# Kernel optimization log

Hardware: AMD Instinct MI355X
Metric: run time of the kernel (lower is better)

## Reference

```python
import jax, jax.numpy as jnp
import numpy as np

B, N, K = 2, 8192, 16
C_IN, C_OUT, HID = 64, 256, 256
L, HEADS, DKQV = 2, 8, 32
D = HEADS * DKQV  # 256


def setup_inputs() -> dict:
    key = jax.random.key(0)
    ks = jax.random.split(key, 20)
    s = 0.02
    inp = {
        "xyzs": jax.random.normal(ks[0], (B, N, 3), jnp.float32),
        "features": jax.random.normal(ks[1], (B, N, C_IN), jnp.float32),
        "k_graph": jax.random.randint(ks[2], (B, N, K), 0, N),
        "W_in": jax.random.normal(ks[3], (C_IN, HID), jnp.float32) * s,
        "b_in": jnp.zeros((HID,), jnp.float32),
        "Wq": jax.random.normal(ks[4], (L, HID, D), jnp.float32) * s,
        "bq": jnp.zeros((L, D), jnp.float32),
        "Wk": jax.random.normal(ks[5], (L, HID, D), jnp.float32) * s,
        "bk": jnp.zeros((L, D), jnp.float32),
        "Wv": jax.random.normal(ks[6], (L, HID, D), jnp.float32) * s,
        "bv": jnp.zeros((L, D), jnp.float32),
        "Wp": jax.random.normal(ks[7], (L, 3, D), jnp.float32) * s,
        "bp": jnp.zeros((L, D), jnp.float32),
        "Wo": jax.random.normal(ks[8], (L, D, HID), jnp.float32) * s,
        "bo": jnp.zeros((L, HID), jnp.float32),
        "W_out": jax.random.normal(ks[9], (HID, C_OUT), jnp.float32) * s,
        "b_out": jnp.zeros((C_OUT,), jnp.float32),
    }
    return inp


def _gather(f, idx):
    # f: [B,N,D], idx: [B,N,K] -> [B,N,K,D]
    return jnp.take_along_axis(f[:, None], idx[..., None], axis=2)


def _knn_attn(xyz, f, idx, Wq, bq, Wk, bk, Wv, bv, Wp, bp, Wo, bo):
    b, n, _ = f.shape
    q = f @ Wq + bq                      # [B,N,D]
    k = f @ Wk + bk
    v = f @ Wv + bv
    k_nb = _gather(k, idx)               # [B,N,K,D]
    v_nb = _gather(v, idx)
    rel = xyz[:, :, None, :] - _gather(xyz, idx)   # [B,N,K,3]
    pos = rel @ Wp + bp                  # [B,N,K,D] relative positional encoding
    kh = (k_nb + pos).reshape(b, n, K, HEADS, DKQV)
    vh = (v_nb + pos).reshape(b, n, K, HEADS, DKQV)
    qh = q.reshape(b, n, HEADS, DKQV)
    logits = jnp.einsum('bnhd,bnkhd->bnhk', qh, kh) / np.sqrt(DKQV)
    attn = jax.nn.softmax(logits, axis=-1)          # softmax over K neighbors
    o = jnp.einsum('bnhk,bnkhd->bnhd', attn, vh).reshape(b, n, D)
    return o @ Wo + bo


def reference(xyzs, features, k_graph, W_in, b_in, Wq, bq, Wk, bk, Wv, bv,
              Wp, bp, Wo, bo, W_out, b_out):
    f = features @ W_in + b_in
    for l in range(L):
        res = f  # res_connection=True
        f = _knn_attn(xyzs, f, k_graph, Wq[l], bq[l], Wk[l], bk[l],
                      Wv[l], bv[l], Wp[l], bp[l], Wo[l], bo[l]) + res
    out = f @ W_out + b_out
    return jax.nn.leaky_relu(out, negative_slope=0.01)
```

## Files before the change

### kernel.cpp

```cpp
#include <hip/hip_runtime.h>
#include <hip/hip_bf16.h>

typedef __attribute__((ext_vector_type(8))) short bf16x8;
typedef __attribute__((ext_vector_type(4))) float f32x4;
typedef unsigned int uint;

constexpr int NPTS = 8192;
constexpr int BPTS = 16384;
constexpr int KNN  = 16;

__device__ __forceinline__ void gload16(const void* g, void* l) {
    __builtin_amdgcn_global_load_lds(
        (const __attribute__((address_space(1))) unsigned int*)g,
        (__attribute__((address_space(3))) unsigned int*)l, 16, 0, 0);
}

__device__ __forceinline__ float2 bf2f2(uint u) {
    float2 r;
    r.x = __uint_as_float(u << 16);
    r.y = __uint_as_float(u & 0xffff0000u);
    return r;
}

__device__ __forceinline__ uint packbf2(float a, float b) {
    union { __hip_bfloat16 h; unsigned short u; } ua, ub;
    ua.h = __float2bfloat16(a); ub.h = __float2bfloat16(b);
    return (uint)ua.u | ((uint)ub.u << 16);
}

template<int KD, bool RES, bool OUTF32, bool LRELU>
__global__ __launch_bounds__(256) void gemm_mfma(
    const __hip_bfloat16* __restrict__ A,
    const __hip_bfloat16* __restrict__ Bt,
    const float* __restrict__ b0, const float* __restrict__ b1,
    const float* __restrict__ b2,
    const __hip_bfloat16* __restrict__ res,
    void* __restrict__ Cout, int M, int N)
{
    __shared__ __align__(16) __hip_bfloat16 As[128 * 64];
    __shared__ __align__(16) __hip_bfloat16 Bs[128 * 64];

    const int tid  = threadIdx.x;
    const int lane = tid & 63;
    const int wid  = tid >> 6;
    const int wm   = (wid >> 1) * 64;
    const int wn   = (wid & 1) * 64;
    const int bm   = blockIdx.y * 128;
    const int bn   = blockIdx.x * 128;

    const int srow8 = lane >> 3;
    const int sslot = (lane & 7) ^ srow8;

    const int r = lane & 15;
    const int g = lane >> 4;

    f32x4 acc[4][4] = {};

    for (int k0 = 0; k0 < KD; k0 += 64) {
        #pragma unroll
        for (int p = 0; p < 4; ++p) {
            const int rowA = p * 32 + wid * 8 + srow8;
            gload16(&A[(size_t)(bm + rowA) * KD + k0 + sslot * 8],
                    (char*)As + (p * 32 + wid * 8) * 128);
            gload16(&Bt[(size_t)(bn + rowA) * KD + k0 + sslot * 8],
                    (char*)Bs + (p * 32 + wid * 8) * 128);
        }
        __syncthreads();

        bf16x8 af[2][4], bfr[2][4];
        #pragma unroll
        for (int s = 0; s < 2; ++s) {
            const int physA = (s * 4 + g) ^ (r & 7);
            #pragma unroll
            for (int mi = 0; mi < 4; ++mi)
                af[s][mi] = *(const bf16x8*)((const char*)As + (wm + mi * 16 + r) * 128 + physA * 16);
            #pragma unroll
            for (int ni = 0; ni < 4; ++ni)
                bfr[s][ni] = *(const bf16x8*)((const char*)Bs + (wn + ni * 16 + r) * 128 + physA * 16);
        }
        #pragma unroll
        for (int s = 0; s < 2; ++s)
            #pragma unroll
            for (int mi = 0; mi < 4; ++mi)
                #pragma unroll
                for (int ni = 0; ni < 4; ++ni)
                    acc[mi][ni] = __builtin_amdgcn_mfma_f32_16x16x32_bf16(
                        af[s][mi], bfr[s][ni], acc[mi][ni], 0, 0, 0);
        __syncthreads();
    }

    #pragma unroll
    for (int ni = 0; ni < 4; ++ni) {
        const int col = bn + wn + ni * 16 + r;
        const float* bsel = (col < 256) ? b0 : (col < 512 ? b1 : b2);
        const float bias = bsel[col & 255];
        #pragma unroll
        for (int mi = 0; mi < 4; ++mi) {
            #pragma unroll
            for (int q = 0; q < 4; ++q) {
                const int row = bm + wm + mi * 16 + g * 4 + q;
                float v = acc[mi][ni][q] + bias;
                if (RES)  v += __bfloat162float(res[(size_t)row * N + col]);
                if (LRELU) v = v > 0.f ? v : 0.01f * v;
                if (OUTF32) ((float*)Cout)[(size_t)row * N + col] = v;
                else ((__hip_bfloat16*)Cout)[(size_t)row * N + col] = __float2bfloat16(v);
            }
        }
    }
}

__global__ __launch_bounds__(256) void prep_kernel(
    const float* __restrict__ W_in, const float* __restrict__ Wq,
    const float* __restrict__ Wk,  const float* __restrict__ Wv,
    const float* __restrict__ Wo,  const float* __restrict__ W_out,
    const float* __restrict__ features,
    __hip_bfloat16* __restrict__ WtIn,  __hip_bfloat16* __restrict__ WtQKV,
    __hip_bfloat16* __restrict__ WtO,   __hip_bfloat16* __restrict__ WtOut,
    __hip_bfloat16* __restrict__ featb)
{
    const int b = blockIdx.x;
    if (b < 592) {
        const float* srcs[10] = {W_in, Wq, Wk, Wv, Wq + 65536, Wk + 65536,
                                 Wv + 65536, Wo, Wo + 65536, W_out};
        __hip_bfloat16* dsts[10] = {
            WtIn, WtQKV, WtQKV + 65536, WtQKV + 131072,
            WtQKV + 196608, WtQKV + 262144, WtQKV + 327680,
            WtO, WtO + 65536, WtOut};
        const int Ks[10]    = {64,256,256,256,256,256,256,256,256,256};
        const int start[10] = {0,16,80,144,208,272,336,400,464,528};
        int j = 0;
        #pragma unroll
        for (int i = 1; i < 10; ++i) if (b >= start[i]) j = i;
        const int t  = b - start[j];
        const int Kd = Ks[j];
        const int ntk = Kd >> 5;
        const int tn = t / ntk;
        const int tk = t - tn * ntk;

        __shared__ float s[32][33];
        const int tx = threadIdx.x & 31, ty = threadIdx.x >> 5;
        const float* src = srcs[j];
        #pragma unroll
        for (int i = 0; i < 4; ++i)
            s[ty + i * 8][tx] = src[(size_t)(tk * 32 + ty + i * 8) * 256 + tn * 32 + tx];
        __syncthreads();
        __hip_bfloat16* dst = dsts[j];
        #pragma unroll
        for (int i = 0; i < 4; ++i)
            dst[(size_t)(tn * 32 + ty + i * 8) * Kd + tk * 32 + tx] =
                __float2bfloat16(s[tx][ty + i * 8]);
    } else {
        const int i = (b - 592) * 1024 + threadIdx.x * 4;
        const float4 v = *(const float4*)&features[i];
        __hip_bfloat16 tmp[4] = {__float2bfloat16(v.x), __float2bfloat16(v.y),
                                 __float2bfloat16(v.z), __float2bfloat16(v.w)};
        *(uint2*)&featb[i] = *(const uint2*)tmp;
    }
}

__global__ __launch_bounds__(256) void knn_attn_kernel(
    const float* __restrict__ xyz,
    const int*   __restrict__ idx,
    const __hip_bfloat16* __restrict__ qkv,
    const float* __restrict__ Wp,
    const float* __restrict__ bp,
    __hip_bfloat16* __restrict__ o)
{
    const int tid = threadIdx.x;
    const int pt  = tid >> 7;
    const int lt  = tid & 127;
    const int p0  = blockIdx.x * 2;
    const int p   = p0 + pt;

    __shared__ int   s_row[2][KNN];
    __shared__ float s_rel[2][KNN][3];
    __shared__ float s_wq[2][8][4];
    __shared__ float s_attn[2][8][KNN];
    __shared__ float s_arel[2][8][3];
    __shared__ __align__(16) __hip_bfloat16 v_lds[2][KNN][256];

    if (tid < 32) {
        const int pp = tid >> 4;
        const int kk = tid & 15;
        const int pg = p0 + pp;
        const int bidx = pg >> 13;
        const int j = idx[pg * KNN + kk];
        const int jrow = (bidx << 13) + j;
        s_row[pp][kk] = jrow;
        s_rel[pp][kk][0] = xyz[pg * 3 + 0] - xyz[jrow * 3 + 0];
        s_rel[pp][kk][1] = xyz[pg * 3 + 1] - xyz[jrow * 3 + 1];
        s_rel[pp][kk][2] = xyz[pg * 3 + 2] - xyz[jrow * 3 + 2];
    } else if (tid >= 64 && tid < 128) {
        const int t2 = tid - 64;
        const int pp = t2 >> 5;
        const int hh = (t2 >> 2) & 7;
        const int j  = t2 & 3;
        const __hip_bfloat16* qrow = qkv + (size_t)(p0 + pp) * 768 + hh * 32;
        const float* w = (j < 3) ? (Wp + j * 256 + hh * 32) : (bp + hh * 32);
        float acc = 0.f;
        #pragma unroll
        for (int c = 0; c < 32; c += 2) {
            const float2 qf = bf2f2(*(const uint*)&qrow[c]);
            acc += qf.x * w[c] + qf.y * w[c + 1];
        }
        s_wq[pp][hh][j] = acc;
    }
    __syncthreads();

    {
        const int wv  = tid >> 6, ln = tid & 63;
        const int ptw = wv >> 1;
        const int rb  = (wv & 1) * 8;
        #pragma unroll
        for (int c = 0; c < 4; ++c) {
            const int kk = rb + c * 2 + (ln >> 5);
            const int jr = s_row[ptw][kk];
            gload16(qkv + (size_t)jr * 768 + 512 + (ln & 31) * 8,
                    (char*)&v_lds[ptw][rb + c * 2][0]);
        }
    }

    const int h = lt >> 4;
    const int k = lt & 15;
    {
        const int jrow = s_row[pt][k];
        const uint4* qp = (const uint4*)(qkv + (size_t)p * 768 + h * 32);
        const uint4* kp = (const uint4*)(qkv + (size_t)jrow * 768 + 256 + h * 32);
        float dot = 0.f;
        #pragma unroll
        for (int i = 0; i < 4; ++i) {
            const uint4 qu = qp[i], ku = kp[i];
            float2 qf, kf;
            qf = bf2f2(qu.x); kf = bf2f2(ku.x); dot += qf.x * kf.x + qf.y * kf.y;
            qf = bf2f2(qu.y); kf = bf2f2(ku.y); dot += qf.x * kf.x + qf.y * kf.y;
            qf = bf2f2(qu.z); kf = bf2f2(ku.z); dot += qf.x * kf.x + qf.y * kf.y;
            qf = bf2f2(qu.w); kf = bf2f2(ku.w); dot += qf.x * kf.x + qf.y * kf.y;
        }
        const float r0 = s_rel[pt][k][0], r1 = s_rel[pt][k][1], r2 = s_rel[pt][k][2];
        const float logit = (dot + r0 * s_wq[pt][h][0] + r1 * s_wq[pt][h][1]
                                 + r2 * s_wq[pt][h][2] + s_wq[pt][h][3])
                            * 0.1767766952966369f;
        float mx = logit;
        #pragma unroll
        for (int off = 8; off >= 1; off >>= 1)
            mx = fmaxf(mx, __shfl_xor(mx, off, 16));
        const float e = __expf(logit - mx);
        float den = e;
        #pragma unroll
        for (int off = 8; off >= 1; off >>= 1)
            den += __shfl_xor(den, off, 16);
        const float attn = e / den;
        s_attn[pt][h][k] = attn;

        float a0 = attn * r0, a1 = attn * r1, a2 = attn * r2;
        #pragma unroll
        for (int off = 8; off >= 1; off >>= 1) {
            a0 += __shfl_xor(a0, off, 16);
            a1 += __shfl_xor(a1, off, 16);
            a2 += __shfl_xor(a2, off, 16);
        }
        if (k == 0) {
            s_arel[pt][h][0] = a0;
            s_arel[pt][h][1] = a1;
            s_arel[pt][h][2] = a2;
        }
    }
    __syncthreads();

    {
        const int ch = lt * 2;
        float ax = 0.f, ay = 0.f;
        #pragma unroll
        for (int kk = 0; kk < KNN; ++kk) {
            const float a = s_attn[pt][h][kk];
            const float2 vf = bf2f2(*(const uint*)&v_lds[pt][kk][ch]);
            ax += a * vf.x;
            ay += a * vf.y;
        }
        const float2 wp0 = *(const float2*)&Wp[ch];
        const float2 wp1 = *(const float2*)&Wp[256 + ch];
        const float2 wp2 = *(const float2*)&Wp[512 + ch];
        const float2 bpv = *(const float2*)&bp[ch];
        const float r0 = s_arel[pt][h][0], r1 = s_arel[pt][h][1], r2 = s_arel[pt][h][2];
        ax += r0 * wp0.x + r1 * wp1.x + r2 * wp2.x + bpv.x;
        ay += r0 * wp0.y + r1 * wp1.y + r2 * wp2.y + bpv.y;
        *(uint*)&o[(size_t)p * 256 + ch] = packbf2(ax, ay);
    }
}

extern "C" void kernel_launch(void* const* d_in, const int* in_sizes, int n_in,
                              void* d_out, int out_size, void* d_ws, size_t ws_size,
                              hipStream_t stream)
{
    const float* xyzs     = (const float*)d_in[0];
    const float* features = (const float*)d_in[1];
    const int*   k_graph  = (const int*)  d_in[2];
    const float* W_in     = (const float*)d_in[3];
    const float* b_in     = (const float*)d_in[4];
    const float* Wq       = (const float*)d_in[5];
    const float* bq       = (const float*)d_in[6];
    const float* Wk       = (const float*)d_in[7];
    const float* bk       = (const float*)d_in[8];
    const float* Wv       = (const float*)d_in[9];
    const float* bv       = (const float*)d_in[10];
    const float* Wp       = (const float*)d_in[11];
    const float* bp       = (const float*)d_in[12];
    const float* Wo       = (const float*)d_in[13];
    const float* bo       = (const float*)d_in[14];
    const float* W_out    = (const float*)d_in[15];
    const float* b_out    = (const float*)d_in[16];

    __hip_bfloat16* featb = (__hip_bfloat16*)d_ws;
    __hip_bfloat16* f     = featb + 1048576;
    __hip_bfloat16* qkv   = f + 4194304;
    __hip_bfloat16* ob    = qkv + 12582912;
    __hip_bfloat16* WtIn  = ob + 4194304;
    __hip_bfloat16* WtQKV = WtIn + 16384;
    __hip_bfloat16* WtO   = WtQKV + 393216;
    __hip_bfloat16* WtOut = WtO + 131072;

    prep_kernel<<<1616, 256, 0, stream>>>(W_in, Wq, Wk, Wv, Wo, W_out, features,
                                          WtIn, WtQKV, WtO, WtOut, featb);

    gemm_mfma<64, false, false, false><<<dim3(2, 128), 256, 0, stream>>>(
        featb, WtIn, b_in, b_in, b_in, nullptr, f, BPTS, 256);

    for (int l = 0; l < 2; ++l) {
        gemm_mfma<256, false, false, false><<<dim3(6, 128), 256, 0, stream>>>(
            f, WtQKV + (size_t)l * 196608,
            bq + l * 256, bk + l * 256, bv + l * 256, nullptr, qkv, BPTS, 768);

        knn_attn_kernel<<<dim3(BPTS / 2), 256, 0, stream>>>(
            xyzs, k_graph, qkv, Wp + (size_t)l * 768, bp + l * 256, ob);

        gemm_mfma<256, true, false, false><<<dim3(2, 128), 256, 0, stream>>>(
            ob, WtO + (size_t)l * 65536,
            bo + l * 256, bo + l * 256, bo + l * 256, f, f, BPTS, 256);
    }

    gemm_mfma<256, false, true, true><<<dim3(2, 128), 256, 0, stream>>>(
        f, WtOut, b_out, b_out, b_out, nullptr, (float*)d_out, BPTS, 256);
}
```

Baseline: 151.9 us.

## Store QKV as fp16 and use packed fdot2 in kNN attention

The QKV GEMM now writes fp16 instead of bf16, and Wp/bp are pre-converted to fp16 in the prep kernel. The attention kernel uses v_dot2 fp16 instructions for the q·k and q·Wp dot products in place of scalar bf16 unpacking. Neighbor index lookup, q/k loads and V prefetch into LDS are issued before the first barrier, removing the shared s_row staging and a barrier round-trip. The trade-off is fp16 range and precision for the QKV activations, plus redundant index loads per thread.

```diff
diff --git a/kernel.cpp b/kernel.cpp
--- a/kernel.cpp
+++ b/kernel.cpp
@@ -3,6 +3,8 @@
 
 typedef __attribute__((ext_vector_type(8))) short bf16x8;
 typedef __attribute__((ext_vector_type(4))) float f32x4;
+typedef __attribute__((ext_vector_type(2))) _Float16 h2;
+typedef __attribute__((ext_vector_type(8))) _Float16 h8;
 typedef unsigned int uint;
 
 constexpr int NPTS = 8192;
@@ -15,20 +17,13 @@
         (__attribute__((address_space(3))) unsigned int*)l, 16, 0, 0);
 }
 
-__device__ __forceinline__ float2 bf2f2(uint u) {
-    float2 r;
-    r.x = __uint_as_float(u << 16);
-    r.y = __uint_as_float(u & 0xffff0000u);
-    return r;
-}
-
 __device__ __forceinline__ uint packbf2(float a, float b) {
     union { __hip_bfloat16 h; unsigned short u; } ua, ub;
     ua.h = __float2bfloat16(a); ub.h = __float2bfloat16(b);
     return (uint)ua.u | ((uint)ub.u << 16);
 }
 
-template<int KD, bool RES, bool OUTF32, bool LRELU>
+template<int KD, bool RES, int OUTT, bool LRELU>
 __global__ __launch_bounds__(256) void gemm_mfma(
     const __hip_bfloat16* __restrict__ A,
     const __hip_bfloat16* __restrict__ Bt,
@@ -50,7 +45,6 @@
 
     const int srow8 = lane >> 3;
     const int sslot = (lane & 7) ^ srow8;
-
     const int r = lane & 15;
     const int g = lane >> 4;
 
@@ -102,8 +96,9 @@
                 float v = acc[mi][ni][q] + bias;
                 if (RES)  v += __bfloat162float(res[(size_t)row * N + col]);
                 if (LRELU) v = v > 0.f ? v : 0.01f * v;
-                if (OUTF32) ((float*)Cout)[(size_t)row * N + col] = v;
-                else ((__hip_bfloat16*)Cout)[(size_t)row * N + col] = __float2bfloat16(v);
+                if (OUTT == 0)      ((float*)Cout)[(size_t)row * N + col] = v;
+                else if (OUTT == 1) ((__hip_bfloat16*)Cout)[(size_t)row * N + col] = __float2bfloat16(v);
+                else                ((_Float16*)Cout)[(size_t)row * N + col] = (_Float16)v;
             }
         }
     }
@@ -114,9 +109,10 @@
     const float* __restrict__ Wk,  const float* __restrict__ Wv,
     const float* __restrict__ Wo,  const float* __restrict__ W_out,
     const float* __restrict__ features,
+    const float* __restrict__ Wp,  const float* __restrict__ bp,
     __hip_bfloat16* __restrict__ WtIn,  __hip_bfloat16* __restrict__ WtQKV,
     __hip_bfloat16* __restrict__ WtO,   __hip_bfloat16* __restrict__ WtOut,
-    __hip_bfloat16* __restrict__ featb)
+    __hip_bfloat16* __restrict__ featb, _Float16* __restrict__ Wpb)
 {
     const int b = blockIdx.x;
     if (b < 592) {
@@ -149,21 +145,32 @@
         for (int i = 0; i < 4; ++i)
             dst[(size_t)(tn * 32 + ty + i * 8) * Kd + tk * 32 + tx] =
                 __float2bfloat16(s[tx][ty + i * 8]);
-    } else {
+    } else if (b < 1616) {
         const int i = (b - 592) * 1024 + threadIdx.x * 4;
         const float4 v = *(const float4*)&features[i];
         __hip_bfloat16 tmp[4] = {__float2bfloat16(v.x), __float2bfloat16(v.y),
                                  __float2bfloat16(v.z), __float2bfloat16(v.w)};
         *(uint2*)&featb[i] = *(const uint2*)tmp;
+    } else {
+        const int e8 = threadIdx.x * 8;
+        const int l  = e8 >> 10;
+        const int rr = (e8 >> 8) & 3;
+        const int c  = e8 & 255;
+        const float* src = (rr < 3) ? (Wp + (size_t)l * 768 + rr * 256 + c)
+                                    : (bp + (size_t)l * 256 + c);
+        const float4 f0 = ((const float4*)src)[0];
+        const float4 f1 = ((const float4*)src)[1];
+        _Float16 t[8] = {(_Float16)f0.x, (_Float16)f0.y, (_Float16)f0.z, (_Float16)f0.w,
+                         (_Float16)f1.x, (_Float16)f1.y, (_Float16)f1.z, (_Float16)f1.w};
+        *(uint4*)&Wpb[(size_t)l * 1024 + rr * 256 + c] = *(const uint4*)t;
     }
 }
 
 __global__ __launch_bounds__(256) void knn_attn_kernel(
     const float* __restrict__ xyz,
     const int*   __restrict__ idx,
-    const __hip_bfloat16* __restrict__ qkv,
-    const float* __restrict__ Wp,
-    const float* __restrict__ bp,
+    const _Float16* __restrict__ qkv,
+    const _Float16* __restrict__ Wpb,
     __hip_bfloat16* __restrict__ o)
 {
     const int tid = threadIdx.x;
@@ -171,99 +178,94 @@
     const int lt  = tid & 127;
     const int p0  = blockIdx.x * 2;
     const int p   = p0 + pt;
-
-    __shared__ int   s_row[2][KNN];
+    const int h   = lt >> 4;
+    const int k   = lt & 15;
+
     __shared__ float s_rel[2][KNN][3];
     __shared__ float s_wq[2][8][4];
     __shared__ float s_attn[2][8][KNN];
     __shared__ float s_arel[2][8][3];
-    __shared__ __align__(16) __hip_bfloat16 v_lds[2][KNN][256];
+    __shared__ __align__(16) _Float16 v_lds[2][KNN][256];
+
+    const int jrow = ((p >> 13) << 13) + idx[p * KNN + k];
+    const h8* qp = (const h8*)(qkv + (size_t)p * 768 + h * 32);
+    const h8* kp = (const h8*)(qkv + (size_t)jrow * 768 + 256 + h * 32);
+    const h8 q0 = qp[0], q1 = qp[1];
+    const h8 k0 = kp[0], k1 = kp[1];
+
+    {
+        const int w = tid >> 6, ln = tid & 63;
+        #pragma unroll
+        for (int c = 0; c < 4; ++c) {
+            const int grE = w * 8 + c * 2;
+            const int gr  = grE + (ln >> 5);
+            const int ptw = grE >> 4, kkE = grE & 15;
+            const int pg  = p0 + (gr >> 4);
+            const int jr  = ((pg >> 13) << 13) + idx[pg * KNN + (gr & 15)];
+            gload16(qkv + (size_t)jr * 768 + 512 + (ln & 31) * 8,
+                    (char*)&v_lds[ptw][kkE][0]);
+        }
+    }
 
     if (tid < 32) {
-        const int pp = tid >> 4;
-        const int kk = tid & 15;
+        const int pp = tid >> 4, kk = tid & 15;
         const int pg = p0 + pp;
-        const int bidx = pg >> 13;
-        const int j = idx[pg * KNN + kk];
-        const int jrow = (bidx << 13) + j;
-        s_row[pp][kk] = jrow;
-        s_rel[pp][kk][0] = xyz[pg * 3 + 0] - xyz[jrow * 3 + 0];
-        s_rel[pp][kk][1] = xyz[pg * 3 + 1] - xyz[jrow * 3 + 1];
-        s_rel[pp][kk][2] = xyz[pg * 3 + 2] - xyz[jrow * 3 + 2];
-    } else if (tid >= 64 && tid < 128) {
-        const int t2 = tid - 64;
-        const int pp = t2 >> 5;
-        const int hh = (t2 >> 2) & 7;
-        const int j  = t2 & 3;
-        const __hip_bfloat16* qrow = qkv + (size_t)(p0 + pp) * 768 + hh * 32;
-        const float* w = (j < 3) ? (Wp + j * 256 + hh * 32) : (bp + hh * 32);
+        const int jr = ((pg >> 13) << 13) + idx[pg * KNN + kk];
+        s_rel[pp][kk][0] = xyz[pg * 3 + 0] - xyz[jr * 3 + 0];
+        s_rel[pp][kk][1] = xyz[pg * 3 + 1] - xyz[jr * 3 + 1];
+        s_rel[pp][kk][2] = xyz[pg * 3 + 2] - xyz[jr * 3 + 2];
+    } else if (tid < 96) {
+        const int t2 = tid - 32;
+        const int pp = t2 >> 5, hh = (t2 >> 2) & 7, j = t2 & 3;
+        const h8* qr = (const h8*)(qkv + (size_t)(p0 + pp) * 768 + hh * 32);
+        const h8* wr = (const h8*)(Wpb + j * 256 + hh * 32);
+        const h8 a0 = qr[0], a1 = qr[1], b0 = wr[0], b1 = wr[1];
         float acc = 0.f;
         #pragma unroll
-        for (int c = 0; c < 32; c += 2) {
-            const float2 qf = bf2f2(*(const uint*)&qrow[c]);
-            acc += qf.x * w[c] + qf.y * w[c + 1];
-        }
+        for (int i = 0; i < 4; ++i)
+            acc = __builtin_amdgcn_fdot2(((const h2*)&a0)[i], ((const h2*)&b0)[i], acc, false);
+        #pragma unroll
+        for (int i = 0; i < 4; ++i)
+            acc = __builtin_amdgcn_fdot2(((const h2*)&a1)[i], ((const h2*)&b1)[i], acc, false);
         s_wq[pp][hh][j] = acc;
     }
+
+    float dot = 0.f;
+    #pragma unroll
+    for (int i = 0; i < 4; ++i)
+        dot = __builtin_amdgcn_fdot2(((const h2*)&q0)[i], ((const h2*)&k0)[i], dot, false);
+    #pragma unroll
+    for (int i = 0; i < 4; ++i)
+        dot = __builtin_amdgcn_fdot2(((const h2*)&q1)[i], ((const h2*)&k1)[i], dot, false);
     __syncthreads();
 
-    {
-        const int wv  = tid >> 6, ln = tid & 63;
-        const int ptw = wv >> 1;
-        const int rb  = (wv & 1) * 8;
-        #pragma unroll
-        for (int c = 0; c < 4; ++c) {
-            const int kk = rb + c * 2 + (ln >> 5);
-            const int jr = s_row[ptw][kk];
-            gload16(qkv + (size_t)jr * 768 + 512 + (ln & 31) * 8,
-                    (char*)&v_lds[ptw][rb + c * 2][0]);
-        }
-    }
-
-    const int h = lt >> 4;
-    const int k = lt & 15;
-    {
-        const int jrow = s_row[pt][k];
-        const uint4* qp = (const uint4*)(qkv + (size_t)p * 768 + h * 32);
-        const uint4* kp = (const uint4*)(qkv + (size_t)jrow * 768 + 256 + h * 32);
-        float dot = 0.f;
-        #pragma unroll
-        for (int i = 0; i < 4; ++i) {
-            const uint4 qu = qp[i], ku = kp[i];
-            float2 qf, kf;
-            qf = bf2f2(qu.x); kf = bf2f2(ku.x); dot += qf.x * kf.x + qf.y * kf.y;
-            qf = bf2f2(qu.y); kf = bf2f2(ku.y); dot += qf.x * kf.x + qf.y * kf.y;
-            qf = bf2f2(qu.z); kf = bf2f2(ku.z); dot += qf.x * kf.x + qf.y * kf.y;
-            qf = bf2f2(qu.w); kf = bf2f2(ku.w); dot += qf.x * kf.x + qf.y * kf.y;
-        }
-        const float r0 = s_rel[pt][k][0], r1 = s_rel[pt][k][1], r2 = s_rel[pt][k][2];
-        const float logit = (dot + r0 * s_wq[pt][h][0] + r1 * s_wq[pt][h][1]
-                                 + r2 * s_wq[pt][h][2] + s_wq[pt][h][3])
-                            * 0.1767766952966369f;
-        float mx = logit;
-        #pragma unroll
-        for (int off = 8; off >= 1; off >>= 1)
-            mx = fmaxf(mx, __shfl_xor(mx, off, 16));
-        const float e = __expf(logit - mx);
-        float den = e;
-        #pragma unroll
-        for (int off = 8; off >= 1; off >>= 1)
-            den += __shfl_xor(den, off, 16);
-        const float attn = e / den;
-        s_attn[pt][h][k] = attn;
-
-        float a0 = attn * r0, a1 = attn * r1, a2 = attn * r2;
-        #pragma unroll
-        for (int off = 8; off >= 1; off >>= 1) {
-            a0 += __shfl_xor(a0, off, 16);
-            a1 += __shfl_xor(a1, off, 16);
-            a2 += __shfl_xor(a2, off, 16);
-        }
-        if (k == 0) {
-            s_arel[pt][h][0] = a0;
-            s_arel[pt][h][1] = a1;
-            s_arel[pt][h][2] = a2;
-        }
+    const float r0 = s_rel[pt][k][0], r1 = s_rel[pt][k][1], r2 = s_rel[pt][k][2];
+    const float logit = (dot + r0 * s_wq[pt][h][0] + r1 * s_wq[pt][h][1]
+                             + r2 * s_wq[pt][h][2] + s_wq[pt][h][3])
+                        * 0.1767766952966369f;
+    float mx = logit;
+    #pragma unroll
+    for (int off = 8; off >= 1; off >>= 1)
+        mx = fmaxf(mx, __shfl_xor(mx, off, 16));
+    const float e = __expf(logit - mx);
+    float den = e;
+    #pragma unroll
+    for (int off = 8; off >= 1; off >>= 1)
+        den += __shfl_xor(den, off, 16);
+    const float attn = e / den;
+    s_attn[pt][h][k] = attn;
+
+    float a0 = attn * r0, a1 = attn * r1, a2 = attn * r2;
+    #pragma unroll
+    for (int off = 8; off >= 1; off >>= 1) {
+        a0 += __shfl_xor(a0, off, 16);
+        a1 += __shfl_xor(a1, off, 16);
+        a2 += __shfl_xor(a2, off, 16);
+    }
+    if (k == 0) {
+        s_arel[pt][h][0] = a0;
+        s_arel[pt][h][1] = a1;
+        s_arel[pt][h][2] = a2;
     }
     __syncthreads();
 
@@ -273,17 +275,17 @@
         #pragma unroll
         for (int kk = 0; kk < KNN; ++kk) {
             const float a = s_attn[pt][h][kk];
-            const float2 vf = bf2f2(*(const uint*)&v_lds[pt][kk][ch]);
-            ax += a * vf.x;
-            ay += a * vf.y;
-        }
-        const float2 wp0 = *(const float2*)&Wp[ch];
-        const float2 wp1 = *(const float2*)&Wp[256 + ch];
-        const float2 wp2 = *(const float2*)&Wp[512 + ch];
-        const float2 bpv = *(const float2*)&bp[ch];
-        const float r0 = s_arel[pt][h][0], r1 = s_arel[pt][h][1], r2 = s_arel[pt][h][2];
-        ax += r0 * wp0.x + r1 * wp1.x + r2 * wp2.x + bpv.x;
-        ay += r0 * wp0.y + r1 * wp1.y + r2 * wp2.y + bpv.y;
+            const h2 vf = *(const h2*)&v_lds[pt][kk][ch];
+            ax += a * (float)vf.x;
+            ay += a * (float)vf.y;
+        }
+        const h2 w0 = *(const h2*)&Wpb[ch];
+        const h2 w1 = *(const h2*)&Wpb[256 + ch];
+        const h2 w2 = *(const h2*)&Wpb[512 + ch];
+        const h2 w3 = *(const h2*)&Wpb[768 + ch];
+        const float g0 = s_arel[pt][h][0], g1 = s_arel[pt][h][1], g2 = s_arel[pt][h][2];
+        ax += g0 * (float)w0.x + g1 * (float)w1.x + g2 * (float)w2.x + (float)w3.x;
+        ay += g0 * (float)w0.y + g1 * (float)w1.y + g2 * (float)w2.y + (float)w3.y;
         *(uint*)&o[(size_t)p * 256 + ch] = packbf2(ax, ay);
     }
 }
@@ -312,32 +314,34 @@
 
     __hip_bfloat16* featb = (__hip_bfloat16*)d_ws;
     __hip_bfloat16* f     = featb + 1048576;
-    __hip_bfloat16* qkv   = f + 4194304;
-    __hip_bfloat16* ob    = qkv + 12582912;
+    _Float16*       qkv   = (_Float16*)(f + 4194304);
+    __hip_bfloat16* ob    = (__hip_bfloat16*)(qkv + 12582912);
     __hip_bfloat16* WtIn  = ob + 4194304;
     __hip_bfloat16* WtQKV = WtIn + 16384;
     __hip_bfloat16* WtO   = WtQKV + 393216;
     __hip_bfloat16* WtOut = WtO + 131072;
-
-    prep_kernel<<<1616, 256, 0, stream>>>(W_in, Wq, Wk, Wv, Wo, W_out, features,
-                                          WtIn, WtQKV, WtO, WtOut, featb);
-
-    gemm_mfma<64, false, false, false><<<dim3(2, 128), 256, 0, stream>>>(
+    _Float16*       Wpb   = (_Float16*)(WtOut + 65536);
+
+    prep_kernel<<<1617, 256, 0, stream>>>(W_in, Wq, Wk, Wv, Wo, W_out, features,
+                                          Wp, bp, WtIn, WtQKV, WtO, WtOut,
+                                          featb, Wpb);
+
+    gemm_mfma<64, false, 1, false><<<dim3(2, 128), 256, 0, stream>>>(
         featb, WtIn, b_in, b_in, b_in, nullptr, f, BPTS, 256);
 
     for (int l = 0; l < 2; ++l) {
-        gemm_mfma<256, false, false, false><<<dim3(6, 128), 256, 0, stream>>>(
+        gemm_mfma<256, false, 2, false><<<dim3(6, 128), 256, 0, stream>>>(
             f, WtQKV + (size_t)l * 196608,
             bq + l * 256, bk + l * 256, bv + l * 256, nullptr, qkv, BPTS, 768);
 
         knn_attn_kernel<<<dim3(BPTS / 2), 256, 0, stream>>>(
-            xyzs, k_graph, qkv, Wp + (size_t)l * 768, bp + l * 256, ob);
-
-        gemm_mfma<256, true, false, false><<<dim3(2, 128), 256, 0, stream>>>(
+            xyzs, k_graph, qkv, Wpb + (size_t)l * 1024, ob);
+
+        gemm_mfma<256, true, 1, false><<<dim3(2, 128), 256, 0, stream>>>(
             ob, WtO + (size_t)l * 65536,
             bo + l * 256, bo + l * 256, bo + l * 256, f, f, BPTS, 256);
     }
 
-    gemm_mfma<256, false, true, true><<<dim3(2, 128), 256, 0, stream>>>(
+    gemm_mfma<256, false, 0, true><<<dim3(2, 128), 256, 0, stream>>>(
         f, WtOut, b_out, b_out, b_out, nullptr, (float*)d_out, BPTS, 256);
 }
```

Measured after the change: 131.6 us. -13.4%, faster.
